# Performance work log

Measured on AMD Instinct MI355X. Metric: run time of the kernel, lower is better.

The kernel has to match this reference:

```python
import jax, jax.numpy as jnp
import numpy as np

B, T, F, H, L, K, LAB = 512, 128, 256, 384, 3, 10, 25
CH = H // L            # chunk_size = 128
GATES = 4 * H + 2 * L  # 1542


def _cumax_l2r(x):
    return jnp.cumsum(jax.nn.softmax(x, -1), -1)


def _cumax_r2l(x):
    # softmax is permutation-equivariant: softmax(flip(x)) == flip(softmax(x))
    s = jax.nn.softmax(x, -1)
    return jnp.flip(jnp.cumsum(jnp.flip(s, -1), -1), -1)


def setup_inputs() -> dict:
    key = jax.random.key(0)
    ks = jax.random.split(key, 16)
    s = 0.05
    return {
        "X": jax.random.normal(ks[0], (B, T, F), jnp.float32),
        "v_lengths": jax.random.randint(ks[1], (B,), 1, T + 1),
        "kernel_w": jax.random.normal(ks[2], (F + 1, GATES), jnp.float32) * s,
        "kernel_b": jnp.zeros((GATES,), jnp.float32),
        "rec_w": jax.random.normal(ks[3], (H + 1, GATES), jnp.float32) * s,
        "rec_b": jnp.zeros((GATES,), jnp.float32),
        "scale_w": jax.random.normal(ks[4], (H, H // 6), jnp.float32) * s,
        "scale_b": jnp.zeros((H // 6,), jnp.float32),
        "rescale_w": jax.random.normal(ks[5], (H // 6, H), jnp.float32) * s,
        "rescale_b": jnp.zeros((H,), jnp.float32),
        "conv_w": jax.random.normal(ks[6], (H, H, K), jnp.float32) * s,  # (out_ch, in_ch, kernel)
        "conv_b": jnp.zeros((H,), jnp.float32),
        "out_w": jax.random.normal(ks[7], (H, LAB), jnp.float32) * s,
        "out_b": jnp.zeros((LAB,), jnp.float32),
    }


def reference(X, v_lengths, kernel_w, kernel_b, rec_w, rec_b, scale_w, scale_b,
              rescale_w, rescale_b, conv_w, conv_b, out_w, out_b):
    # time interval T: ones with T[:,0]=0 (no timestamps provided)
    Tint = jnp.ones((B, T), X.dtype).at[:, 0].set(0.0)

    def step(carry, xs):
        c, h, tmp_h, tmp_dis = carry       # c,h: (B,H); tmp_h: (K,B,H); tmp_dis: (K,B)
        x_t, t_t = xs                      # (B,F), (B,)
        xo = (jnp.concatenate([x_t, t_t[:, None]], -1) @ kernel_w + kernel_b
              + jnp.concatenate([h, t_t[:, None]], -1) @ rec_w + rec_b)
        fm = _cumax_l2r(xo[:, :L])         # (B,L)
        im = _cumax_r2l(xo[:, L:2 * L])    # (B,L)
        g = xo[:, 2 * L:].reshape(B, 4 * L, CH)
        f_g = jax.nn.sigmoid(g[:, :L])
        i_g = jax.nn.sigmoid(g[:, L:2 * L])
        o_g = jax.nn.sigmoid(g[:, 2 * L:3 * L])
        c_in = jnp.tanh(g[:, 3 * L:])
        c_l = c.reshape(B, L, CH)
        fm3, im3 = fm[:, :, None], im[:, :, None]
        ov = fm3 * im3
        c_new = ov * (f_g * c_l + i_g * c_in) + (fm3 - ov) * c_l + (im3 - ov) * c_in
        h_new = (o_g * jnp.tanh(c_new)).reshape(B, H)
        c_new = c_new.reshape(B, H)
        cur_dist = 1.0 - jnp.mean(fm, -1)  # (B,)
        tmp_h = jnp.concatenate([tmp_h[1:], h_new[None]], 0)
        tmp_dis = jnp.concatenate([tmp_dis[1:], cur_dist[None]], 0)
        local_dis = jax.nn.softmax(jnp.cumsum(tmp_dis.T, axis=1), axis=1)  # (B,K)
        local_h = tmp_h.transpose(1, 2, 0) * local_dis[:, None, :]          # (B,H,K)
        theme = jnp.mean(local_h, -1)                                       # (B,H)
        theme = jax.nn.sigmoid(
            jax.nn.relu(theme @ scale_w + scale_b) @ rescale_w + rescale_b)
        conv = jnp.einsum('bhk,ohk->bo', local_h, conv_w) + conv_b          # (B,H)
        return (c_new, h_new, tmp_h, tmp_dis), (h_new, theme * conv)

    init = (jnp.zeros((B, H), X.dtype), jnp.zeros((B, H), X.dtype),
            jnp.zeros((K, B, H), X.dtype), jnp.zeros((K, B), X.dtype))
    _, (origin_h, h_seq) = jax.lax.scan(step, init, (X.transpose(1, 0, 2), Tint.T))
    # origin_h, h_seq: (T,B,H). dropout layers in eval mode -> identity.
    rnn = h_seq + origin_h
    out = rnn @ out_w + out_b                                  # (T,B,LAB)
    cur_mask = (jnp.arange(T)[None, :] == (v_lengths - 1)[:, None]).astype(X.dtype)
    cur_output = jnp.einsum('tbl,bt->bl', out, cur_mask)       # (B,LAB)
    return cur_output
```

## Files before the change

kernel.cpp:

```cpp
#include <hip/hip_runtime.h>
#include <hip/hip_bf16.h>

constexpr int kB = 512, kT = 128, kF = 256, kH = 384, kK = 10, kLab = 25;
constexpr int kGates = 1542;
constexpr int kNsw = 1552;
constexpr int kWstride = 392;
constexpr int kSstride = 194;

typedef short bf16x8 __attribute__((ext_vector_type(8)));
typedef float f32x4 __attribute__((ext_vector_type(4)));

__device__ __forceinline__ float sigm(float x) { return 1.f / (1.f + __expf(-x)); }

__device__ __forceinline__ unsigned short bf16bits(float x) {
  __hip_bfloat16 h = __float2bfloat16(x);
  return __builtin_bit_cast(unsigned short, h);
}

__device__ __forceinline__ int swcol_orig(int sc) {
  int ns = sc / 192, lc = sc % 192, w = lc / 48, wc = lc % 48;
  int g = wc / 12, jj = ns * 48 + w * 12 + wc % 12;
  int l = jj >> 7, ch = jj & 127;
  return 6 + (g * 3 + l) * 128 + ch;
}

__global__ void prep_kernel(const float* __restrict__ kernel_w,
                            const float* __restrict__ kernel_b,
                            const float* __restrict__ rec_w,
                            const float* __restrict__ rec_b,
                            const float* __restrict__ conv_w,
                            __hip_bfloat16* __restrict__ Wr_lin,
                            __hip_bfloat16* __restrict__ Wlog,
                            __hip_bfloat16* __restrict__ Wx_sw,
                            __hip_bfloat16* __restrict__ W2sw,
                            float* __restrict__ bias,
                            __hip_bfloat16* __restrict__ Hh,
                            int* __restrict__ Cnt) {
  const long ntot = 1474560;
  const long stride = (long)gridDim.x * blockDim.x;
  for (long i = (long)blockIdx.x * blockDim.x + threadIdx.x; i < ntot; i += stride) {
    {
      int j = (int)(i & 31);
      long r = i >> 5;
      int n = (int)(r % 384);
      int c = (int)(r / 384);
      int kk = c * 32 + j;
      int kc = kk / 384, h = kk % 384;
      W2sw[i] = __float2bfloat16(conv_w[((long)n * 384 + h) * 10 + kc]);
    }
    if (i < 589824) {
      int sc = (int)(i / 384), k = (int)(i % 384);
      Wr_lin[i] = __float2bfloat16(rec_w[(long)k * kGates + swcol_orig(sc)]);
    }
    if (i < 397312) {
      int j = (int)(i & 31);
      long r = i >> 5;
      int n = (int)(r % kNsw);
      int c = (int)(r / kNsw);
      int k = c * 32 + j;
      int col = (n < 1536) ? swcol_orig(n) : ((n < 1542) ? (n - 1536) : -1);
      Wx_sw[i] = (col >= 0) ? __float2bfloat16(kernel_w[(long)k * kGates + col])
                            : __float2bfloat16(0.f);
    }
    if (i < 6144) {
      int j = (int)(i & 31);
      long r = i >> 5;
      int n = (int)(r % 16);
      int c = (int)(r / 16);
      int k = c * 32 + j;
      Wlog[i] = (n < 6) ? __float2bfloat16(rec_w[(long)k * kGates + n])
                        : __float2bfloat16(0.f);
    }
    if (i < kGates) {
      float b0 = kernel_b[i] + rec_b[i];
      bias[i] = b0;
      bias[kGates + i] = b0 + kernel_w[(long)kF * kGates + i] + rec_w[(long)kH * kGates + i];
    }
    if (i < (long)kB * kH) Hh[i] = __float2bfloat16(0.f);
    if (i < 1024) Cnt[i] = 0;
  }
}

__global__ __launch_bounds__(256) void xw_kernel(const float* __restrict__ X,
                                                 const __hip_bfloat16* __restrict__ Wx_sw,
                                                 __hip_bfloat16* __restrict__ XW) {
  const int tid = threadIdx.x;
  const int lane = tid & 63, wave = tid >> 6;
  const int r16 = lane & 15, quad = lane >> 4;
  const int m0 = blockIdx.x * 64 + wave * 16;
  const int m = m0 + r16;
  const int t = m >> 9, b = m & 511;
  const float* xrow = X + ((size_t)b * kT + t) * kF;

  bf16x8 a[8];
#pragma unroll
  for (int c = 0; c < 8; ++c) {
    float4 p0 = *(const float4*)(xrow + c * 32 + quad * 8);
    float4 p1 = *(const float4*)(xrow + c * 32 + quad * 8 + 4);
    union { bf16x8 v; __hip_bfloat16 h[8]; } u;
    u.h[0] = __float2bfloat16(p0.x); u.h[1] = __float2bfloat16(p0.y);
    u.h[2] = __float2bfloat16(p0.z); u.h[3] = __float2bfloat16(p0.w);
    u.h[4] = __float2bfloat16(p1.x); u.h[5] = __float2bfloat16(p1.y);
    u.h[6] = __float2bfloat16(p1.z); u.h[7] = __float2bfloat16(p1.w);
    a[c] = u.v;
  }
  for (int tile = 0; tile < 97; ++tile) {
    f32x4 acc = (f32x4){0.f, 0.f, 0.f, 0.f};
#pragma unroll
    for (int c = 0; c < 8; ++c) {
      bf16x8 bf = *(const bf16x8*)(Wx_sw + ((size_t)c * kNsw + tile * 16 + r16) * 32 + quad * 8);
      acc = __builtin_amdgcn_mfma_f32_16x16x32_bf16(a[c], bf, acc, 0, 0, 0);
    }
#pragma unroll
    for (int r = 0; r < 4; ++r)
      XW[(size_t)(m0 + quad * 4 + r) * kNsw + tile * 16 + r16] = __float2bfloat16(acc[r]);
  }
}

__global__ __launch_bounds__(256, 1) void step_all(
    const __hip_bfloat16* __restrict__ Wr_lin, const __hip_bfloat16* __restrict__ Wlog,
    const float* __restrict__ bias, const __hip_bfloat16* __restrict__ XW,
    __hip_bfloat16* __restrict__ Hh, float* __restrict__ Dhist,
    int* __restrict__ Cnt) {
  extern __shared__ char smem[];
  __hip_bfloat16* Wl = (__hip_bfloat16*)smem;
  float* scratch = (float*)(smem + 150528);
  float* Lg = (float*)(smem + 162944);
  float* fmS = (float*)(smem + 163328);
  float* imS = (float*)(smem + 163584);

  const int bx = blockIdx.x;
  const int mt = bx >> 3, ns = bx & 7;
  const int tid = threadIdx.x;
  const int lane = tid & 63, wave = tid >> 6;
  const int r16 = lane & 15, quad = lane >> 4;
  const int brow = mt * 16 + r16;
  int* cnt = Cnt + mt * 32;

  {
    const __hip_bfloat16* src = Wr_lin + (size_t)ns * 192 * 384;
    for (int i = tid; i < 192 * 384 / 8; i += 256) {
      int lc = (i * 8) / 384, k = (i * 8) % 384;
      *(bf16x8*)(Wl + lc * kWstride + k) = *(const bf16x8*)(src + i * 8);
    }
  }
  __syncthreads();

  float creg[4] = {0.f, 0.f, 0.f, 0.f};

  for (int step = 0; step < kT; ++step) {
    const float* bt = bias + (step > 0 ? kGates : 0);

    const __hip_bfloat16* XWrow = XW + (size_t)(step * kB + mt * 16) * kNsw;
    float xwv[3][4];
#pragma unroll
    for (int t3 = 0; t3 < 3; ++t3) {
      int col = ns * 192 + wave * 48 + t3 * 16 + r16;
#pragma unroll
      for (int r = 0; r < 4; ++r)
        xwv[t3][r] = __bfloat162float(XWrow[(size_t)(quad * 4 + r) * kNsw + col]);
    }
    float xlv[4] = {0.f, 0.f, 0.f, 0.f};
    if (wave == 0) {
#pragma unroll
      for (int r = 0; r < 4; ++r)
        xlv[r] = __bfloat162float(XWrow[(size_t)(quad * 4 + r) * kNsw + 1536 + r16]);
    }

    if (step > 0) {
      if (tid == 0) {
        const int target = 8 * step;
        while (__hip_atomic_load(cnt, __ATOMIC_RELAXED, __HIP_MEMORY_SCOPE_AGENT) < target) {
        }
      }
      __syncthreads();
    }

    bf16x8 a[12];
    {
      unsigned long long* Hq =
          (unsigned long long*)(Hh + ((size_t)step * kB + brow) * kH);
#pragma unroll
      for (int c = 0; c < 12; ++c) {
        union { unsigned long long q[2]; bf16x8 v; } u;
        u.q[0] = __hip_atomic_load(&Hq[c * 8 + quad * 2], __ATOMIC_RELAXED,
                                   __HIP_MEMORY_SCOPE_AGENT);
        u.q[1] = __hip_atomic_load(&Hq[c * 8 + quad * 2 + 1], __ATOMIC_RELAXED,
                                   __HIP_MEMORY_SCOPE_AGENT);
        a[c] = u.v;
      }
    }

    f32x4 acc[3];
#pragma unroll
    for (int t3 = 0; t3 < 3; ++t3) {
#pragma unroll
      for (int r = 0; r < 4; ++r) acc[t3][r] = xwv[t3][r];
    }
    f32x4 accL = (f32x4){xlv[0], xlv[1], xlv[2], xlv[3]};

#pragma unroll
    for (int c = 0; c < 12; ++c) {
#pragma unroll
      for (int t3 = 0; t3 < 3; ++t3) {
        bf16x8 bf = *(const bf16x8*)(Wl + (wave * 48 + t3 * 16 + r16) * kWstride + c * 32 + quad * 8);
        acc[t3] = __builtin_amdgcn_mfma_f32_16x16x32_bf16(a[c], bf, acc[t3], 0, 0, 0);
      }
      if (wave == 0) {
        bf16x8 bfl = *(const bf16x8*)(Wlog + ((size_t)c * 16 + r16) * 32 + quad * 8);
        accL = __builtin_amdgcn_mfma_f32_16x16x32_bf16(a[c], bfl, accL, 0, 0, 0);
      }
    }

    if (wave == 0 && r16 < 6) {
#pragma unroll
      for (int r = 0; r < 4; ++r) Lg[(quad * 4 + r) * 6 + r16] = accL[r] + bt[r16];
    }
#pragma unroll
    for (int t3 = 0; t3 < 3; ++t3) {
      int colb = wave * 48 + t3 * 16 + r16;
#pragma unroll
      for (int r = 0; r < 4; ++r) scratch[(quad * 4 + r) * kSstride + colb] = acc[t3][r];
    }
    __syncthreads();

    if (tid < 16) {
      float z0 = Lg[tid * 6 + 0], z1 = Lg[tid * 6 + 1], z2 = Lg[tid * 6 + 2];
      float m = fmaxf(z0, fmaxf(z1, z2));
      float e0 = __expf(z0 - m), e1 = __expf(z1 - m), e2 = __expf(z2 - m);
      float inv = 1.f / (e0 + e1 + e2);
      float fm0 = e0 * inv, fm1 = (e0 + e1) * inv, fm2 = 1.f;
      float z3 = Lg[tid * 6 + 3], z4 = Lg[tid * 6 + 4], z5 = Lg[tid * 6 + 5];
      float m2 = fmaxf(z3, fmaxf(z4, z5));
      float e3 = __expf(z3 - m2), e4 = __expf(z4 - m2), e5 = __expf(z5 - m2);
      float inv2 = 1.f / (e3 + e4 + e5);
      fmS[tid * 4 + 0] = fm0; fmS[tid * 4 + 1] = fm1; fmS[tid * 4 + 2] = fm2;
      imS[tid * 4 + 0] = 1.f;
      imS[tid * 4 + 1] = (e4 + e5) * inv2;
      imS[tid * 4 + 2] = e5 * inv2;
      if (ns == 0)
        Dhist[(size_t)step * kB + mt * 16 + tid] = 1.f - (fm0 + fm1 + fm2) * (1.f / 3.f);
    }
    __syncthreads();

    unsigned int* HoutU = (unsigned int*)(Hh + (size_t)(step + 1) * kB * kH);
#pragma unroll
    for (int it = 0; it < 2; ++it) {
      int p = tid + it * 256;
      if (p < 384) {
        int row = p & 15, cp = p >> 4;
        float hv[2];
#pragma unroll
        for (int e = 0; e < 2; ++e) {
          int jj = cp * 2 + e;
          int w2 = jj / 12, m12 = jj % 12;
          int lc = w2 * 48 + m12;
          int j = ns * 48 + jj;
          int l = j >> 7, ch = j & 127;
          float gf = scratch[row * kSstride + lc]      + bt[6 + (0 * 3 + l) * 128 + ch];
          float gi = scratch[row * kSstride + lc + 12] + bt[6 + (1 * 3 + l) * 128 + ch];
          float go = scratch[row * kSstride + lc + 24] + bt[6 + (2 * 3 + l) * 128 + ch];
          float gc = scratch[row * kSstride + lc + 36] + bt[6 + (3 * 3 + l) * 128 + ch];
          float fg = sigm(gf), ig = sigm(gi), og = sigm(go), ci = tanhf(gc);
          float fm = fmS[row * 4 + l], im = imS[row * 4 + l], ov = fm * im;
          float c0 = creg[it * 2 + e];
          float c1 = ov * (fg * c0 + ig * ci) + (fm - ov) * c0 + (im - ov) * ci;
          creg[it * 2 + e] = c1;
          hv[e] = og * tanhf(c1);
        }
        unsigned int packed =
            (unsigned int)bf16bits(hv[0]) | ((unsigned int)bf16bits(hv[1]) << 16);
        size_t eidx = ((size_t)(mt * 16 + row) * kH + ns * 48 + cp * 2) >> 1;
        __hip_atomic_store(&HoutU[eidx], packed, __ATOMIC_RELAXED,
                           __HIP_MEMORY_SCOPE_AGENT);
      }
    }

    asm volatile("s_waitcnt vmcnt(0)" ::: "memory");
    __syncthreads();
    if (tid == 0)
      __hip_atomic_fetch_add(cnt, 1, __ATOMIC_RELAXED, __HIP_MEMORY_SCOPE_AGENT);
  }
}

__global__ void epi1_kernel(const int* __restrict__ vlen,
                            const float* __restrict__ Dhist,
                            const __hip_bfloat16* __restrict__ Hh,
                            __hip_bfloat16* __restrict__ Zbf, float* __restrict__ theme,
                            float* __restrict__ hbase) {
  int b = blockIdx.x, tid = threadIdx.x;
  int tb = vlen[b] - 1;
  float d[kK], ld[kK];
  float run = 0.f;
#pragma unroll
  for (int k = 0; k < kK; ++k) {
    int s = tb - (kK - 1) + k;
    float dv = (s >= 0) ? Dhist[(size_t)s * kB + b] : 0.f;
    run += dv;
    d[k] = run;
  }
  float m = d[0];
#pragma unroll
  for (int k = 1; k < kK; ++k) m = fmaxf(m, d[k]);
  float se = 0.f;
#pragma unroll
  for (int k = 0; k < kK; ++k) { ld[k] = __expf(d[k] - m); se += ld[k]; }
  float inv = 1.f / se;
#pragma unroll
  for (int k = 0; k < kK; ++k) ld[k] *= inv;

  for (int h = tid; h < kH; h += blockDim.x) {
    float th = 0.f;
#pragma unroll
    for (int k = 0; k < kK; ++k) {
      int s = tb - (kK - 1) + k;
      float hv = (s >= 0) ? __bfloat162float(Hh[((size_t)(s + 1) * kB + b) * kH + h]) : 0.f;
      float z = ld[k] * hv;
      Zbf[(size_t)b * (kK * kH) + k * kH + h] = __float2bfloat16(z);
      th += z;
    }
    theme[(size_t)b * kH + h] = th * (1.f / kK);
    hbase[(size_t)b * kH + h] = __bfloat162float(Hh[((size_t)(tb + 1) * kB + b) * kH + h]);
  }
}

__global__ void epi2_kernel(const float* __restrict__ theme,
                            const float* __restrict__ scale_w,
                            const float* __restrict__ scale_b, float* __restrict__ U) {
  int b = blockIdx.x, o = threadIdx.x;
  __shared__ float tr[kH];
  for (int h = o; h < kH; h += 64) tr[h] = theme[(size_t)b * kH + h];
  __syncthreads();
  float a = scale_b[o];
  for (int h = 0; h < kH; ++h) a += tr[h] * scale_w[(size_t)h * 64 + o];
  U[(size_t)b * 64 + o] = fmaxf(a, 0.f);
}

__global__ void epi3_kernel(const float* __restrict__ U,
                            const float* __restrict__ rescale_w,
                            const float* __restrict__ rescale_b, float* __restrict__ V) {
  int b = blockIdx.x, tid = threadIdx.x;
  __shared__ float ur[64];
  if (tid < 64) ur[tid] = U[(size_t)b * 64 + tid];
  __syncthreads();
  for (int o = tid; o < kH; o += 128) {
    float a = rescale_b[o];
#pragma unroll
    for (int k = 0; k < 64; ++k) a += ur[k] * rescale_w[(size_t)k * kH + o];
    V[(size_t)b * kH + o] = sigm(a);
  }
}

__global__ __launch_bounds__(256) void epi4m_kernel(const __hip_bfloat16* __restrict__ Zbf,
                                                    const __hip_bfloat16* __restrict__ W2sw,
                                                    const float* __restrict__ conv_b,
                                                    float* __restrict__ ConvO) {
  const int mt = blockIdx.x, nh = blockIdx.y;
  const int tid = threadIdx.x;
  const int lane = tid & 63, wave = tid >> 6;
  const int r16 = lane & 15, quad = lane >> 4;
  const int brow = mt * 16 + r16;
  const int n0w = nh * 192 + wave * 48;
  const __hip_bfloat16* Zrow = Zbf + (size_t)brow * (kK * kH);
  f32x4 acc[3];
#pragma unroll
  for (int t3 = 0; t3 < 3; ++t3) acc[t3] = (f32x4){0.f, 0.f, 0.f, 0.f};
  for (int c = 0; c < 120; ++c) {
    bf16x8 a = *(const bf16x8*)(Zrow + c * 32 + quad * 8);
#pragma unroll
    for (int t3 = 0; t3 < 3; ++t3) {
      bf16x8 bf = *(const bf16x8*)(W2sw + ((size_t)c * kH + n0w + t3 * 16 + r16) * 32 + quad * 8);
      acc[t3] = __builtin_amdgcn_mfma_f32_16x16x32_bf16(a, bf, acc[t3], 0, 0, 0);
    }
  }
#pragma unroll
  for (int t3 = 0; t3 < 3; ++t3) {
    int col = n0w + t3 * 16 + r16;
#pragma unroll
    for (int r = 0; r < 4; ++r)
      ConvO[(size_t)(mt * 16 + quad * 4 + r) * kH + col] = acc[t3][r] + conv_b[col];
  }
}

__global__ void epi5_kernel(const float* __restrict__ V, const float* __restrict__ ConvO,
                            const float* __restrict__ hbase,
                            const float* __restrict__ out_w,
                            const float* __restrict__ out_b, float* __restrict__ out) {
  int b = blockIdx.x, tid = threadIdx.x;
  __shared__ float r[kH];
  for (int h = tid; h < kH; h += 64)
    r[h] = V[(size_t)b * kH + h] * ConvO[(size_t)b * kH + h] + hbase[(size_t)b * kH + h];
  __syncthreads();
  if (tid < kLab) {
    float a = out_b[tid];
    for (int h = 0; h < kH; ++h) a += r[h] * out_w[(size_t)h * kLab + tid];
    out[(size_t)b * kLab + tid] = a;
  }
}

extern "C" void kernel_launch(void* const* d_in, const int* in_sizes, int n_in,
                              void* d_out, int out_size, void* d_ws, size_t ws_size,
                              hipStream_t stream) {
  (void)in_sizes; (void)n_in; (void)out_size; (void)ws_size;
  const float* X = (const float*)d_in[0];
  const int* vlen = (const int*)d_in[1];
  const float* kernel_w = (const float*)d_in[2];
  const float* kernel_b = (const float*)d_in[3];
  const float* rec_w = (const float*)d_in[4];
  const float* rec_b = (const float*)d_in[5];
  const float* scale_w = (const float*)d_in[6];
  const float* scale_b = (const float*)d_in[7];
  const float* rescale_w = (const float*)d_in[8];
  const float* rescale_b = (const float*)d_in[9];
  const float* conv_w = (const float*)d_in[10];
  const float* conv_b = (const float*)d_in[11];
  const float* out_w = (const float*)d_in[12];
  const float* out_b = (const float*)d_in[13];
  float* out = (float*)d_out;

  char* ws = (char*)d_ws;
  size_t off = 0;
  auto alloc = [&](size_t bytes) -> void* {
    void* p = ws + off;
    off += (bytes + 255) & ~(size_t)255;
    return p;
  };
  __hip_bfloat16* XW = (__hip_bfloat16*)alloc((size_t)kT * kB * kNsw * 2);
  __hip_bfloat16* Hh = (__hip_bfloat16*)alloc((size_t)(kT + 1) * kB * kH * 2);
  __hip_bfloat16* Wr_lin = (__hip_bfloat16*)alloc((size_t)1536 * 384 * 2);
  __hip_bfloat16* Wlog = (__hip_bfloat16*)alloc((size_t)12 * 16 * 32 * 2);
  __hip_bfloat16* Wx_sw = (__hip_bfloat16*)alloc((size_t)8 * kNsw * 32 * 2);
  __hip_bfloat16* W2sw = (__hip_bfloat16*)alloc((size_t)120 * kH * 32 * 2);
  float* bias = (float*)alloc((size_t)2 * kGates * 4);
  float* Dhist = (float*)alloc((size_t)kT * kB * 4);
  __hip_bfloat16* Zbf = (__hip_bfloat16*)alloc((size_t)kB * kK * kH * 2);
  float* theme = (float*)alloc((size_t)kB * kH * 4);
  float* hbase = (float*)alloc((size_t)kB * kH * 4);
  float* U = (float*)alloc((size_t)kB * 64 * 4);
  float* V = (float*)alloc((size_t)kB * kH * 4);
  float* ConvO = (float*)alloc((size_t)kB * kH * 4);
  int* Cnt = (int*)alloc((size_t)1024 * 4);

  hipLaunchKernelGGL(prep_kernel, dim3(1024), dim3(256), 0, stream, kernel_w, kernel_b,
                     rec_w, rec_b, conv_w, Wr_lin, Wlog, Wx_sw, W2sw, bias, Hh, Cnt);

  hipLaunchKernelGGL(xw_kernel, dim3(1024), dim3(256), 0, stream, X, Wx_sw, XW);

  constexpr unsigned kLds = 163840;
  hipFuncSetAttribute((const void*)step_all, hipFuncAttributeMaxDynamicSharedMemorySize,
                      (int)kLds);
  {
    const __hip_bfloat16* a0 = Wr_lin;
    const __hip_bfloat16* a1 = Wlog;
    const float* a2 = bias;
    const __hip_bfloat16* a3 = XW;
    __hip_bfloat16* a4 = Hh;
    float* a5 = Dhist;
    int* a6 = Cnt;
    void* args[] = {&a0, &a1, &a2, &a3, &a4, &a5, &a6};
    hipLaunchCooperativeKernel((const void*)step_all, dim3(256), dim3(256), args, kLds,
                               stream);
  }

  hipLaunchKernelGGL(epi1_kernel, dim3(kB), dim3(128), 0, stream, vlen, Dhist, Hh, Zbf,
                     theme, hbase);
  hipLaunchKernelGGL(epi2_kernel, dim3(kB), dim3(64), 0, stream, theme, scale_w, scale_b, U);
  hipLaunchKernelGGL(epi3_kernel, dim3(kB), dim3(128), 0, stream, U, rescale_w, rescale_b, V);
  hipLaunchKernelGGL(epi4m_kernel, dim3(32, 2), dim3(256), 0, stream, Zbf, W2sw, conv_b,
                     ConvO);
  hipLaunchKernelGGL(epi5_kernel, dim3(kB), dim3(64), 0, stream, V, ConvO, hbase, out_w,
                     out_b, out);
}
```

Before: 1.634 ms.

## Stage recurrent h tile through swizzled LDS, skip step-0 matmul, fast activations

```diff
diff --git a/kernel.cpp b/kernel.cpp
--- a/kernel.cpp
+++ b/kernel.cpp
@@ -10,8 +10,14 @@
 typedef short bf16x8 __attribute__((ext_vector_type(8)));
 typedef float f32x4 __attribute__((ext_vector_type(4)));
 
-__device__ __forceinline__ float sigm(float x) { return 1.f / (1.f + __expf(-x)); }
-
+__device__ __forceinline__ float fast_sigm(float x) {
+  return __builtin_amdgcn_rcpf(1.f + __expf(-x));
+}
+__device__ __forceinline__ float fast_tanh(float x) {
+  x = fminf(fmaxf(x, -15.f), 15.f);
+  float e = __expf(2.f * x);
+  return (e - 1.f) * __builtin_amdgcn_rcpf(e + 1.f);
+}
 __device__ __forceinline__ unsigned short bf16bits(float x) {
   __hip_bfloat16 h = __float2bfloat16(x);
   return __builtin_bit_cast(unsigned short, h);
@@ -124,6 +130,7 @@
     int* __restrict__ Cnt) {
   extern __shared__ char smem[];
   __hip_bfloat16* Wl = (__hip_bfloat16*)smem;
+  char* hbufB = smem + 150528;
   float* scratch = (float*)(smem + 150528);
   float* Lg = (float*)(smem + 162944);
   float* fmS = (float*)(smem + 163328);
@@ -134,7 +141,6 @@
   const int tid = threadIdx.x;
   const int lane = tid & 63, wave = tid >> 6;
   const int r16 = lane & 15, quad = lane >> 4;
-  const int brow = mt * 16 + r16;
   int* cnt = Cnt + mt * 32;
 
   {
@@ -146,7 +152,7 @@
   }
   __syncthreads();
 
-  float creg[4] = {0.f, 0.f, 0.f, 0.f};
+  float creg[2][2] = {{0.f, 0.f}, {0.f, 0.f}};
 
   for (int step = 0; step < kT; ++step) {
     const float* bt = bias + (step > 0 ? kGates : 0);
@@ -167,28 +173,31 @@
         xlv[r] = __bfloat162float(XWrow[(size_t)(quad * 4 + r) * kNsw + 1536 + r16]);
     }
 
+    bf16x8 a[12];
     if (step > 0) {
-      if (tid == 0) {
-        const int target = 8 * step;
-        while (__hip_atomic_load(cnt, __ATOMIC_RELAXED, __HIP_MEMORY_SCOPE_AGENT) < target) {
-        }
+      const int target = 8 * step;
+      while (__hip_atomic_load(cnt, __ATOMIC_RELAXED, __HIP_MEMORY_SCOPE_AGENT) < target) {
+      }
+      const unsigned long long* src = (const unsigned long long*)
+          ((const char*)Hh + (size_t)step * (kB * kH * 2) + (size_t)mt * 12288);
+#pragma unroll
+      for (int pass = 0; pass < 3; ++pass) {
+        int L = pass * 256 + tid;
+        int row = L / 48, c16 = L % 48;
+        union { unsigned long long q[2]; bf16x8 v; } u;
+        u.q[0] = __hip_atomic_load(src + L * 2, __ATOMIC_RELAXED, __HIP_MEMORY_SCOPE_AGENT);
+        u.q[1] = __hip_atomic_load(src + L * 2 + 1, __ATOMIC_RELAXED, __HIP_MEMORY_SCOPE_AGENT);
+        int sw = (c16 & ~7) | ((c16 & 7) ^ (row & 7));
+        *(bf16x8*)(hbufB + row * 768 + sw * 16) = u.v;
       }
       __syncthreads();
-    }
-
-    bf16x8 a[12];
-    {
-      unsigned long long* Hq =
-          (unsigned long long*)(Hh + ((size_t)step * kB + brow) * kH);
 #pragma unroll
       for (int c = 0; c < 12; ++c) {
-        union { unsigned long long q[2]; bf16x8 v; } u;
-        u.q[0] = __hip_atomic_load(&Hq[c * 8 + quad * 2], __ATOMIC_RELAXED,
-                                   __HIP_MEMORY_SCOPE_AGENT);
-        u.q[1] = __hip_atomic_load(&Hq[c * 8 + quad * 2 + 1], __ATOMIC_RELAXED,
-                                   __HIP_MEMORY_SCOPE_AGENT);
-        a[c] = u.v;
+        int c16 = c * 4 + quad;
+        int sw = (c16 & ~7) | ((c16 & 7) ^ (r16 & 7));
+        a[c] = *(const bf16x8*)(hbufB + r16 * 768 + sw * 16);
       }
+      __syncthreads();
     }
 
     f32x4 acc[3];
@@ -199,16 +208,18 @@
     }
     f32x4 accL = (f32x4){xlv[0], xlv[1], xlv[2], xlv[3]};
 
-#pragma unroll
-    for (int c = 0; c < 12; ++c) {
-#pragma unroll
-      for (int t3 = 0; t3 < 3; ++t3) {
-        bf16x8 bf = *(const bf16x8*)(Wl + (wave * 48 + t3 * 16 + r16) * kWstride + c * 32 + quad * 8);
-        acc[t3] = __builtin_amdgcn_mfma_f32_16x16x32_bf16(a[c], bf, acc[t3], 0, 0, 0);
-      }
-      if (wave == 0) {
-        bf16x8 bfl = *(const bf16x8*)(Wlog + ((size_t)c * 16 + r16) * 32 + quad * 8);
-        accL = __builtin_amdgcn_mfma_f32_16x16x32_bf16(a[c], bfl, accL, 0, 0, 0);
+    if (step > 0) {
+#pragma unroll
+      for (int c = 0; c < 12; ++c) {
+#pragma unroll
+        for (int t3 = 0; t3 < 3; ++t3) {
+          bf16x8 bf = *(const bf16x8*)(Wl + (wave * 48 + t3 * 16 + r16) * kWstride + c * 32 + quad * 8);
+          acc[t3] = __builtin_amdgcn_mfma_f32_16x16x32_bf16(a[c], bf, acc[t3], 0, 0, 0);
+        }
+        if (wave == 0) {
+          bf16x8 bfl = *(const bf16x8*)(Wlog + ((size_t)c * 16 + r16) * 32 + quad * 8);
+          accL = __builtin_amdgcn_mfma_f32_16x16x32_bf16(a[c], bfl, accL, 0, 0, 0);
+        }
       }
     }
 
@@ -248,7 +259,7 @@
     for (int it = 0; it < 2; ++it) {
       int p = tid + it * 256;
       if (p < 384) {
-        int row = p & 15, cp = p >> 4;
+        int row = p / 24, cp = p % 24;
         float hv[2];
 #pragma unroll
         for (int e = 0; e < 2; ++e) {
@@ -261,18 +272,18 @@
           float gi = scratch[row * kSstride + lc + 12] + bt[6 + (1 * 3 + l) * 128 + ch];
           float go = scratch[row * kSstride + lc + 24] + bt[6 + (2 * 3 + l) * 128 + ch];
           float gc = scratch[row * kSstride + lc + 36] + bt[6 + (3 * 3 + l) * 128 + ch];
-          float fg = sigm(gf), ig = sigm(gi), og = sigm(go), ci = tanhf(gc);
+          float fg = fast_sigm(gf), ig = fast_sigm(gi);
+          float og = fast_sigm(go), ci = fast_tanh(gc);
           float fm = fmS[row * 4 + l], im = imS[row * 4 + l], ov = fm * im;
-          float c0 = creg[it * 2 + e];
+          float c0 = creg[it][e];
           float c1 = ov * (fg * c0 + ig * ci) + (fm - ov) * c0 + (im - ov) * ci;
-          creg[it * 2 + e] = c1;
-          hv[e] = og * tanhf(c1);
+          creg[it][e] = c1;
+          hv[e] = og * fast_tanh(c1);
         }
         unsigned int packed =
             (unsigned int)bf16bits(hv[0]) | ((unsigned int)bf16bits(hv[1]) << 16);
-        size_t eidx = ((size_t)(mt * 16 + row) * kH + ns * 48 + cp * 2) >> 1;
-        __hip_atomic_store(&HoutU[eidx], packed, __ATOMIC_RELAXED,
-                           __HIP_MEMORY_SCOPE_AGENT);
+        __hip_atomic_store(&HoutU[(size_t)(mt * 16 + row) * 192 + ns * 24 + cp], packed,
+                           __ATOMIC_RELAXED, __HIP_MEMORY_SCOPE_AGENT);
       }
     }
 
@@ -347,7 +358,7 @@
     float a = rescale_b[o];
 #pragma unroll
     for (int k = 0; k < 64; ++k) a += ur[k] * rescale_w[(size_t)k * kH + o];
-    V[(size_t)b * kH + o] = sigm(a);
+    V[(size_t)b * kH + o] = 1.f / (1.f + __expf(-a));
   }
 }
 
```

Measured after the change: 1.308 ms. -20.0%, faster.
